# Performance work log

Hardware: AMD Instinct MI355X
Metric: run time of the kernel (lower is better)

The kernel has to match this reference:

```python
import jax, jax.numpy as jnp
import numpy as np

B, C, H, W = 8, 512, 64, 64
M = C // 8  # query/key channels (scale=8)
EPS = 1e-10
PARAM = 10.0


def elus_feature_map(t):
    # relu branch scaled by PARAM; exp(PARAM * negative part) - 1; +1
    pos = jax.nn.relu(t)
    neg = t - pos
    return PARAM * pos + (jnp.exp(PARAM * neg) - 1.0) + 1.0


def conv1x1(t_flat, Wc, bc):
    # t_flat: [B, Cin, N]; Wc: [Cout, Cin]; bc: [Cout]
    return jnp.einsum('oc,bcn->bon', Wc, t_flat) + bc[None, :, None]


def setup_inputs() -> dict:
    key = jax.random.key(0)
    ks = jax.random.split(key, 16)
    s_in = 1.0 / np.sqrt(C)
    d = dict(
        x=jax.random.normal(ks[0], (B, C, H, W), jnp.float32),
        y=jax.random.normal(ks[1], (B, C, H, W), jnp.float32),
        z=jax.random.normal(ks[2], (B, C, H, W), jnp.float32),
        Wq=jax.random.normal(ks[3], (M, C), jnp.float32) * s_in,
        bq=jnp.zeros((M,), jnp.float32),
        Wk1=jax.random.normal(ks[4], (M, C), jnp.float32) * s_in,
        bk1=jnp.zeros((M,), jnp.float32),
        Wk2=jax.random.normal(ks[5], (M, C), jnp.float32) * s_in,
        bk2=jnp.zeros((M,), jnp.float32),
        Wk3=jax.random.normal(ks[6], (M, C), jnp.float32) * s_in,
        bk3=jnp.zeros((M,), jnp.float32),
        Wv=jax.random.normal(ks[7], (C, C), jnp.float32) * s_in,
        bv=jnp.zeros((C,), jnp.float32),
        Wl=jax.random.normal(ks[8], (C, C), jnp.float32) * s_in,
        bl=jnp.zeros((C,), jnp.float32),
        gamma=jnp.zeros((1,), jnp.float32) + 0.5,  # nonzero so attention path is exercised
    )
    return d


def reference(x, y, z, Wq, bq, Wk1, bk1, Wk2, bk2, Wk3, bk3, Wv, bv, Wl, bl, gamma):
    N = H * W
    xf = x.reshape(B, C, N)
    yf = y.reshape(B, C, N)
    zf = z.reshape(B, C, N)

    Q = elus_feature_map(conv1x1(xf, Wq, bq))      # [B, M, N]
    K = elus_feature_map(conv1x1(xf, Wk1, bk1))    # [B, M, N]
    yK = elus_feature_map(conv1x1(yf, Wk2, bk2))   # [B, M, N]
    zK = elus_feature_map(conv1x1(zf, Wk3, bk3))   # [B, M, N]
    V = conv1x1(xf, Wv, bv)                        # [B, C, N]

    Qn = jnp.swapaxes(Q, 1, 2)                     # [B, N, M]

    def branch(Kb):
        KV = jnp.einsum('bmn,bcn->bmc', Kb, V)                      # [B, M, C]
        norm = 1.0 / jnp.einsum('bnm,bm->bn', Qn, Kb.sum(-1) + EPS)  # [B, N]
        return jnp.einsum('bnm,bmc,bn->bcn', Qn, KV, norm)          # [B, C, N]

    wv = branch(K) + branch(yK) + branch(zK)       # [B, C, N]
    attn = conv1x1(wv, Wl, bl).reshape(B, C, H, W)
    return x + gamma * attn
```

## Files before the change

### kernel.cpp

```cpp
#include <hip/hip_runtime.h>
#include <hip/hip_bf16.h>
#include <math.h>

constexpr int B_ = 8;
constexpr int C_ = 512;
constexpr int M_ = 64;
constexpr int N_ = 4096;
constexpr int NCHUNK_ = 4;
constexpr float EPS_ = 1e-10f;
constexpr float PARAM_ = 10.0f;

typedef __attribute__((ext_vector_type(4))) float f32x4;
typedef __attribute__((ext_vector_type(8))) short bf16x8;

__device__ __forceinline__ float elus(float t) {
    return (t > 0.f) ? fmaf(PARAM_, t, 1.f) : expf(PARAM_ * t);
}

__device__ __forceinline__ short f2bf(float f) {
    return __builtin_bit_cast(short, __float2bfloat16(f));
}
__device__ __forceinline__ float bf2f(short s) {
    unsigned u = ((unsigned)(unsigned short)s) << 16;
    return __builtin_bit_cast(float, u);
}

__global__ __launch_bounds__(256) void prep_w(const float* __restrict__ Wq,
                                              const float* __restrict__ Wk1,
                                              const float* __restrict__ Wk2,
                                              const float* __restrict__ Wk3,
                                              short* __restrict__ Wbf)
{
    int i = blockIdx.x * 256 + threadIdx.x;
    const int MC = M_ * C_;
    if (i < MC) {
        Wbf[i]          = f2bf(Wq[i]);
        Wbf[MC + i]     = f2bf(Wk1[i]);
        Wbf[2 * MC + i] = f2bf(Wk2[i]);
        Wbf[3 * MC + i] = f2bf(Wk3[i]);
    }
}

__global__ __launch_bounds__(256) void feat_mfma(
    const float* __restrict__ x, const float* __restrict__ y,
    const float* __restrict__ z, const short* __restrict__ Wbf,
    const float* __restrict__ bq, const float* __restrict__ bk1,
    const float* __restrict__ bk2, const float* __restrict__ bk3,
    short* __restrict__ QT, short* __restrict__ Kbuf3,
    float* __restrict__ Ksumpart)
{
    const int n0 = blockIdx.x * 64;
    const int which = blockIdx.y;
    const int b  = blockIdx.z;
    const int MC = M_ * C_;

    const float* in = (which == 0) ? x : (which == 1) ? y : z;
    const short* Ws0 = Wbf + (size_t)((which == 0) ? 0 : which + 1) * MC;
    const short* Ws1 = Wbf + (size_t)MC;

    __shared__ short Wlds[2][64][72];
    __shared__ short Xlds[64][72];

    const int tid  = threadIdx.x;
    const int lane = tid & 63;
    const int w    = tid >> 6;
    const int lrow = lane & 15;
    const int lkg  = lane >> 4;

    const float* inb = in + (size_t)b * C_ * N_;

    f32x4 accA[4] = {{0.f,0.f,0.f,0.f},{0.f,0.f,0.f,0.f},{0.f,0.f,0.f,0.f},{0.f,0.f,0.f,0.f}};
    f32x4 accB[4] = {{0.f,0.f,0.f,0.f},{0.f,0.f,0.f,0.f},{0.f,0.f,0.f,0.f},{0.f,0.f,0.f,0.f}};

    const int kq = tid >> 4;
    const int nq = tid & 15;

    for (int kc = 0; kc < C_ / 64; ++kc) {
        const int k0 = kc * 64;
        __syncthreads();
        #pragma unroll
        for (int i = 0; i < 2; ++i) {
            int f = tid + i * 256;
            int r = f >> 3, c8 = (f & 7) * 8;
            *reinterpret_cast<int4*>(&Wlds[0][r][c8]) =
                *reinterpret_cast<const int4*>(&Ws0[(size_t)r * C_ + k0 + c8]);
        }
        if (which == 0) {
            #pragma unroll
            for (int i = 0; i < 2; ++i) {
                int f = tid + i * 256;
                int r = f >> 3, c8 = (f & 7) * 8;
                *reinterpret_cast<int4*>(&Wlds[1][r][c8]) =
                    *reinterpret_cast<const int4*>(&Ws1[(size_t)r * C_ + k0 + c8]);
            }
        }
        f32x4 v0 = *reinterpret_cast<const f32x4*>(&inb[(size_t)(k0 + kq * 4 + 0) * N_ + n0 + nq * 4]);
        f32x4 v1 = *reinterpret_cast<const f32x4*>(&inb[(size_t)(k0 + kq * 4 + 1) * N_ + n0 + nq * 4]);
        f32x4 v2 = *reinterpret_cast<const f32x4*>(&inb[(size_t)(k0 + kq * 4 + 2) * N_ + n0 + nq * 4]);
        f32x4 v3 = *reinterpret_cast<const f32x4*>(&inb[(size_t)(k0 + kq * 4 + 3) * N_ + n0 + nq * 4]);
        #pragma unroll
        for (int c = 0; c < 4; ++c) {
            short4 s;
            s.x = f2bf(v0[c]); s.y = f2bf(v1[c]); s.z = f2bf(v2[c]); s.w = f2bf(v3[c]);
            *reinterpret_cast<short4*>(&Xlds[nq * 4 + c][kq * 4]) = s;
        }
        __syncthreads();
        #pragma unroll
        for (int ks = 0; ks < 2; ++ks) {
            bf16x8 a0 = *reinterpret_cast<const bf16x8*>(&Wlds[0][w * 16 + lrow][ks * 32 + lkg * 8]);
            bf16x8 a1;
            if (which == 0)
                a1 = *reinterpret_cast<const bf16x8*>(&Wlds[1][w * 16 + lrow][ks * 32 + lkg * 8]);
            #pragma unroll
            for (int ns = 0; ns < 4; ++ns) {
                bf16x8 bx = *reinterpret_cast<const bf16x8*>(&Xlds[ns * 16 + lrow][ks * 32 + lkg * 8]);
                accA[ns] = __builtin_amdgcn_mfma_f32_16x16x32_bf16(a0, bx, accA[ns], 0, 0, 0);
                if (which == 0)
                    accB[ns] = __builtin_amdgcn_mfma_f32_16x16x32_bf16(a1, bx, accB[ns], 0, 0, 0);
            }
        }
    }

    auto writeK = [&](const f32x4* acc, const float* bias, int br) {
        short* outb = Kbuf3 + ((size_t)br * B_ + b) * M_ * N_;
        float* ksp  = Ksumpart + ((size_t)br * B_ + b) * 64 * M_;
        #pragma unroll
        for (int r = 0; r < 4; ++r) {
            int m = w * 16 + lkg * 4 + r;
            float bi = bias[m];
            float sv = 0.f;
            #pragma unroll
            for (int ns = 0; ns < 4; ++ns) {
                int n = n0 + ns * 16 + lrow;
                float e = elus(acc[ns][r] + bi);
                outb[(size_t)m * N_ + n] = f2bf(e);
                sv += e;
            }
            sv += __shfl_xor(sv, 1);
            sv += __shfl_xor(sv, 2);
            sv += __shfl_xor(sv, 4);
            sv += __shfl_xor(sv, 8);
            if (lrow == 0)
                ksp[(size_t)blockIdx.x * M_ + m] = sv;
        }
    };

    if (which == 0) {
        short* outb = QT + (size_t)b * N_ * M_;
        int mbase = w * 16 + lkg * 4;
        float bi[4];
        #pragma unroll
        for (int r = 0; r < 4; ++r) bi[r] = bq[mbase + r];
        #pragma unroll
        for (int ns = 0; ns < 4; ++ns) {
            int n = n0 + ns * 16 + lrow;
            short4 s;
            s.x = f2bf(elus(accA[ns][0] + bi[0]));
            s.y = f2bf(elus(accA[ns][1] + bi[1]));
            s.z = f2bf(elus(accA[ns][2] + bi[2]));
            s.w = f2bf(elus(accA[ns][3] + bi[3]));
            *reinterpret_cast<short4*>(&outb[(size_t)n * M_ + mbase]) = s;
        }
        writeK(accB, bk1, 0);
    } else {
        writeK(accA, (which == 1) ? bk2 : bk3, which);
    }
}

__global__ __launch_bounds__(256) void ksum_finalize(const float* __restrict__ Ksumpart,
                                                     float* __restrict__ Ksum)
{
    int i = blockIdx.x * 256 + threadIdx.x;
    if (i >= 3 * B_ * M_) return;
    int br = i / (B_ * M_);
    int rem = i - br * (B_ * M_);
    int b = rem >> 6, m = rem & 63;
    const float* ksp = Ksumpart + ((size_t)br * B_ + b) * 64 * M_;
    float s = 0.f;
    #pragma unroll 8
    for (int nb = 0; nb < 64; ++nb) s += ksp[(size_t)nb * M_ + m];
    Ksum[((size_t)b * 3 + br) * M_ + m] = s;
}

__global__ __launch_bounds__(256) void kx3_mfma(const short* __restrict__ Kbuf3,
                                                const float* __restrict__ x,
                                                float* __restrict__ KXpart3)
{
    const int c0 = blockIdx.x * 32;
    const int nc = blockIdx.y;
    const int b  = blockIdx.z;
    const int nbeg = nc * (N_ / NCHUNK_);

    __shared__ short Klds[3][64][72];
    __shared__ short Xlds[32][72];

    const int tid  = threadIdx.x;
    const int lane = tid & 63;
    const int w    = tid >> 6;
    const int lrow = lane & 15;
    const int lkg  = lane >> 4;

    const float* xb = x + ((size_t)b * C_ + c0) * N_;

    f32x4 acc[3][2] = {};

    for (int it = 0; it < (N_ / NCHUNK_) / 64; ++it) {
        const int n0 = nbeg + it * 64;
        __syncthreads();
        #pragma unroll
        for (int br = 0; br < 3; ++br) {
            const short* kb = Kbuf3 + ((size_t)br * B_ + b) * M_ * N_;
            #pragma unroll
            for (int i = 0; i < 2; ++i) {
                int f = tid + i * 256;
                int r = f >> 3, c8 = (f & 7) * 8;
                *reinterpret_cast<int4*>(&Klds[br][r][c8]) =
                    *reinterpret_cast<const int4*>(&kb[(size_t)r * N_ + n0 + c8]);
            }
        }
        #pragma unroll
        for (int i = 0; i < 2; ++i) {
            int f = tid + i * 256;
            int r = f >> 4, c4 = (f & 15) * 4;
            float4 v = *reinterpret_cast<const float4*>(&xb[(size_t)r * N_ + n0 + c4]);
            short4 s;
            s.x = f2bf(v.x); s.y = f2bf(v.y); s.z = f2bf(v.z); s.w = f2bf(v.w);
            *reinterpret_cast<short4*>(&Xlds[r][c4]) = s;
        }
        __syncthreads();
        #pragma unroll
        for (int s = 0; s < 2; ++s) {
            bf16x8 b0 = *reinterpret_cast<const bf16x8*>(&Xlds[lrow][s * 32 + lkg * 8]);
            bf16x8 b1 = *reinterpret_cast<const bf16x8*>(&Xlds[16 + lrow][s * 32 + lkg * 8]);
            #pragma unroll
            for (int br = 0; br < 3; ++br) {
                bf16x8 a = *reinterpret_cast<const bf16x8*>(&Klds[br][w * 16 + lrow][s * 32 + lkg * 8]);
                acc[br][0] = __builtin_amdgcn_mfma_f32_16x16x32_bf16(a, b0, acc[br][0], 0, 0, 0);
                acc[br][1] = __builtin_amdgcn_mfma_f32_16x16x32_bf16(a, b1, acc[br][1], 0, 0, 0);
            }
        }
    }

    #pragma unroll
    for (int br = 0; br < 3; ++br) {
        float* outp = KXpart3 + (((size_t)br * NCHUNK_ + nc) * B_ + b) * M_ * C_;
        #pragma unroll
        for (int r = 0; r < 4; ++r) {
            int m = w * 16 + lkg * 4 + r;
            outp[(size_t)m * C_ + c0 + lrow]      = acc[br][0][r];
            outp[(size_t)m * C_ + c0 + 16 + lrow] = acc[br][1][r];
        }
    }
}

__global__ __launch_bounds__(256) void kx3_reduce(const float* __restrict__ KXpart3,
                                                  float* __restrict__ KX)
{
    const size_t BMC = (size_t)B_ * M_ * C_;
    size_t i = (size_t)blockIdx.x * 256 + threadIdx.x;
    if (i >= 3 * BMC) return;
    int br = (int)(i / BMC);
    size_t rem = i - (size_t)br * BMC;
    float s = 0.f;
    #pragma unroll
    for (int nc = 0; nc < NCHUNK_; ++nc)
        s += KXpart3[((size_t)br * NCHUNK_ + nc) * BMC + rem];
    size_t b = rem / ((size_t)M_ * C_);
    size_t mc = rem - b * (size_t)M_ * C_;
    KX[((size_t)b * 3 + br) * M_ * C_ + mc] = s;
}

__global__ __launch_bounds__(256) void wlwv_mfma(const float* __restrict__ Wl,
                                                 const float* __restrict__ Wv,
                                                 float* __restrict__ part)
{
    const int k0 = blockIdx.x * 64;
    const int c0 = blockIdx.y * 64;
    const int pc = blockIdx.z;

    __shared__ short Al[64][72];
    __shared__ short Bt[64][72];

    const int tid  = threadIdx.x;
    const int lane = tid & 63;
    const int w    = tid >> 6;
    const int lrow = lane & 15;
    const int lkg  = lane >> 4;
    const int pq = tid >> 4;
    const int nq = tid & 15;

    f32x4 acc[4] = {{0.f,0.f,0.f,0.f},{0.f,0.f,0.f,0.f},{0.f,0.f,0.f,0.f},{0.f,0.f,0.f,0.f}};

    for (int it = 0; it < 2; ++it) {
        const int p0 = pc * 128 + it * 64;
        __syncthreads();
        #pragma unroll
        for (int i = 0; i < 4; ++i) {
            int f = tid + i * 256;
            int r = f >> 4, c4 = (f & 15) * 4;
            f32x4 v = *reinterpret_cast<const f32x4*>(&Wl[(size_t)(c0 + r) * C_ + p0 + c4]);
            short4 s;
            s.x = f2bf(v[0]); s.y = f2bf(v[1]); s.z = f2bf(v[2]); s.w = f2bf(v[3]);
            *reinterpret_cast<short4*>(&Al[r][c4]) = s;
        }
        f32x4 v0 = *reinterpret_cast<const f32x4*>(&Wv[(size_t)(p0 + pq * 4 + 0) * C_ + k0 + nq * 4]);
        f32x4 v1 = *reinterpret_cast<const f32x4*>(&Wv[(size_t)(p0 + pq * 4 + 1) * C_ + k0 + nq * 4]);
        f32x4 v2 = *reinterpret_cast<const f32x4*>(&Wv[(size_t)(p0 + pq * 4 + 2) * C_ + k0 + nq * 4]);
        f32x4 v3 = *reinterpret_cast<const f32x4*>(&Wv[(size_t)(p0 + pq * 4 + 3) * C_ + k0 + nq * 4]);
        #pragma unroll
        for (int c = 0; c < 4; ++c) {
            short4 s;
            s.x = f2bf(v0[c]); s.y = f2bf(v1[c]); s.z = f2bf(v2[c]); s.w = f2bf(v3[c]);
            *reinterpret_cast<short4*>(&Bt[nq * 4 + c][pq * 4]) = s;
        }
        __syncthreads();
        #pragma unroll
        for (int ks = 0; ks < 2; ++ks) {
            bf16x8 a = *reinterpret_cast<const bf16x8*>(&Al[w * 16 + lrow][ks * 32 + lkg * 8]);
            #pragma unroll
            for (int ns = 0; ns < 4; ++ns) {
                bf16x8 bx = *reinterpret_cast<const bf16x8*>(&Bt[ns * 16 + lrow][ks * 32 + lkg * 8]);
                acc[ns] = __builtin_amdgcn_mfma_f32_16x16x32_bf16(a, bx, acc[ns], 0, 0, 0);
            }
        }
    }

    float* pp = part + (size_t)pc * C_ * C_;
    #pragma unroll
    for (int r = 0; r < 4; ++r) {
        int c = c0 + w * 16 + lkg * 4 + r;
        #pragma unroll
        for (int ns = 0; ns < 4; ++ns) {
            int k = k0 + ns * 16 + lrow;
            pp[(size_t)c * C_ + k] = acc[ns][r];
        }
    }
}

__global__ __launch_bounds__(256) void wlwv_reduce(const float* __restrict__ part,
                                                   float* __restrict__ WlWv)
{
    const size_t CC = (size_t)C_ * C_;
    size_t i = (size_t)blockIdx.x * 256 + threadIdx.x;
    if (i >= CC) return;
    float s = 0.f;
    #pragma unroll
    for (int pc = 0; pc < 4; ++pc) s += part[pc * CC + i];
    WlWv[i] = s;
}

__global__ __launch_bounds__(256) void wlbv_kernel(const float* __restrict__ Wl,
                                                   const float* __restrict__ bv,
                                                   float* __restrict__ Wlbv)
{
    int c = blockIdx.x * 256 + threadIdx.x;
    if (c < C_) {
        float s = 0.f;
        for (int p = 0; p < C_; ++p) s = fmaf(Wl[(size_t)c * C_ + p], bv[p], s);
        Wlbv[c] = s;
    }
}

__global__ __launch_bounds__(256) void wfused_mfma(const float* __restrict__ WlWv,
                                                   const float* __restrict__ KX,
                                                   const float* __restrict__ Ksum,
                                                   const float* __restrict__ Wlbv,
                                                   float* __restrict__ Wf)
{
    const int c0 = blockIdx.x * 64;
    const int br = blockIdx.y;
    const int b  = blockIdx.z;

    __shared__ short Al[64][72];
    __shared__ short Bl[64][72];

    const int tid  = threadIdx.x;
    const int lane = tid & 63;
    const int w    = tid >> 6;
    const int lrow = lane & 15;
    const int lkg  = lane >> 4;

    const float* kxb = KX + ((size_t)b * 3 + br) * M_ * C_;

    f32x4 acc[4] = {{0.f,0.f,0.f,0.f},{0.f,0.f,0.f,0.f},{0.f,0.f,0.f,0.f},{0.f,0.f,0.f,0.f}};

    for (int kc = 0; kc < C_ / 64; ++kc) {
        const int k0 = kc * 64;
        __syncthreads();
        #pragma unroll
        for (int i = 0; i < 4; ++i) {
            int f = tid + i * 256;
            int r = f >> 4, c4 = (f & 15) * 4;
            f32x4 v = *reinterpret_cast<const f32x4*>(&WlWv[(size_t)(c0 + r) * C_ + k0 + c4]);
            short4 s;
            s.x = f2bf(v[0]); s.y = f2bf(v[1]); s.z = f2bf(v[2]); s.w = f2bf(v[3]);
            *reinterpret_cast<short4*>(&Al[r][c4]) = s;
        }
        #pragma unroll
        for (int i = 0; i < 4; ++i) {
            int f = tid + i * 256;
            int r = f >> 4, c4 = (f & 15) * 4;
            f32x4 v = *reinterpret_cast<const f32x4*>(&kxb[(size_t)r * C_ + k0 + c4]);
            short4 s;
            s.x = f2bf(v[0]); s.y = f2bf(v[1]); s.z = f2bf(v[2]); s.w = f2bf(v[3]);
            *reinterpret_cast<short4*>(&Bl[r][c4]) = s;
        }
        __syncthreads();
        #pragma unroll
        for (int ks = 0; ks < 2; ++ks) {
            bf16x8 a = *reinterpret_cast<const bf16x8*>(&Al[w * 16 + lrow][ks * 32 + lkg * 8]);
            #pragma unroll
            for (int ns = 0; ns < 4; ++ns) {
                bf16x8 bx = *reinterpret_cast<const bf16x8*>(&Bl[ns * 16 + lrow][ks * 32 + lkg * 8]);
                acc[ns] = __builtin_amdgcn_mfma_f32_16x16x32_bf16(a, bx, acc[ns], 0, 0, 0);
            }
        }
    }

    const float* ks_ = Ksum + ((size_t)b * 3 + br) * M_;
    float* wfb = Wf + (((size_t)b * 3 + br) * C_) * M_;
    #pragma unroll
    for (int r = 0; r < 4; ++r) {
        int c = c0 + w * 16 + lkg * 4 + r;
        float wb = Wlbv[c];
        #pragma unroll
        for (int ns = 0; ns < 4; ++ns) {
            int m = ns * 16 + lrow;
            wfb[(size_t)c * M_ + m] = acc[ns][r] + ks_[m] * wb;
        }
    }
}

__global__ __launch_bounds__(256) void final_mfma_kernel(
    const short* __restrict__ QT, const float* __restrict__ Wf,
    const float* __restrict__ Ksum, const float* __restrict__ x,
    const float* __restrict__ bl, const float* __restrict__ gamma,
    float* __restrict__ out)
{
    const int n0 = blockIdx.x * 64;
    const int c0 = blockIdx.y * 64;
    const int b  = blockIdx.z;

    __shared__ short Qs[64][72];
    __shared__ short Wfs[3][64][72];
    __shared__ float norms[3][64];
    __shared__ float ksef[3][64];

    const int tid  = threadIdx.x;
    const int lane = tid & 63;
    const int w    = tid >> 6;
    const int lrow = lane & 15;
    const int lkg  = lane >> 4;

    const short* qtb = QT + (size_t)b * N_ * M_;
    #pragma unroll
    for (int i = 0; i < 2; ++i) {
        int f = tid + i * 256;
        int r = f >> 3, m8 = (f & 7) * 8;
        *reinterpret_cast<int4*>(&Qs[r][m8]) =
            *reinterpret_cast<const int4*>(&qtb[(size_t)(n0 + r) * M_ + m8]);
    }
    #pragma unroll
    for (int br = 0; br < 3; ++br) {
        const float* wfb = Wf + (((size_t)b * 3 + br) * C_ + c0) * M_;
        #pragma unroll
        for (int i = 0; i < 4; ++i) {
            int f = tid + i * 256;
            int r = f >> 4, m4 = (f & 15) * 4;
            float4 v = *reinterpret_cast<const float4*>(&wfb[(size_t)r * M_ + m4]);
            short4 s;
            s.x = f2bf(v.x); s.y = f2bf(v.y); s.z = f2bf(v.z); s.w = f2bf(v.w);
            *reinterpret_cast<short4*>(&Wfs[br][r][m4]) = s;
        }
    }
    if (tid < 192) {
        int br = tid >> 6, m = tid & 63;
        ksef[br][m] = Ksum[((size_t)b * 3 + br) * M_ + m] + EPS_;
    }
    __syncthreads();
    if (tid < 192) {
        int br = tid >> 6, n = tid & 63;
        float s = 0.f;
        #pragma unroll 16
        for (int m = 0; m < 64; ++m) s = fmaf(bf2f(Qs[n][m]), ksef[br][m], s);
        norms[br][n] = 1.0f / s;
    }
    __syncthreads();

    f32x4 tot[4] = {{0.f,0.f,0.f,0.f},{0.f,0.f,0.f,0.f},{0.f,0.f,0.f,0.f},{0.f,0.f,0.f,0.f}};
    for (int br = 0; br < 3; ++br) {
        f32x4 acc[4] = {{0.f,0.f,0.f,0.f},{0.f,0.f,0.f,0.f},{0.f,0.f,0.f,0.f},{0.f,0.f,0.f,0.f}};
        #pragma unroll
        for (int ks = 0; ks < 2; ++ks) {
            bf16x8 a = *reinterpret_cast<const bf16x8*>(&Wfs[br][w * 16 + lrow][ks * 32 + lkg * 8]);
            #pragma unroll
            for (int ns = 0; ns < 4; ++ns) {
                bf16x8 bq = *reinterpret_cast<const bf16x8*>(&Qs[ns * 16 + lrow][ks * 32 + lkg * 8]);
                acc[ns] = __builtin_amdgcn_mfma_f32_16x16x32_bf16(a, bq, acc[ns], 0, 0, 0);
            }
        }
        #pragma unroll
        for (int ns = 0; ns < 4; ++ns) {
            float nf = norms[br][ns * 16 + lrow];
            #pragma unroll
            for (int r = 0; r < 4; ++r) tot[ns][r] = fmaf(nf, acc[ns][r], tot[ns][r]);
        }
    }

    const float g = gamma[0];
    const float* xb = x + (size_t)b * C_ * N_;
    float* ob = out + (size_t)b * C_ * N_;
    #pragma unroll
    for (int r = 0; r < 4; ++r) {
        int c = c0 + w * 16 + lkg * 4 + r;
        float blc = bl[c];
        #pragma unroll
        for (int ns = 0; ns < 4; ++ns) {
            int n = n0 + ns * 16 + lrow;
            ob[(size_t)c * N_ + n] = fmaf(g, tot[ns][r] + blc, xb[(size_t)c * N_ + n]);
        }
    }
}

extern "C" void kernel_launch(void* const* d_in, const int* in_sizes, int n_in,
                              void* d_out, int out_size, void* d_ws, size_t ws_size,
                              hipStream_t stream)
{
    const float* x   = (const float*)d_in[0];
    const float* y   = (const float*)d_in[1];
    const float* z   = (const float*)d_in[2];
    const float* Wq  = (const float*)d_in[3];
    const float* bq  = (const float*)d_in[4];
    const float* Wk1 = (const float*)d_in[5];
    const float* bk1 = (const float*)d_in[6];
    const float* Wk2 = (const float*)d_in[7];
    const float* bk2 = (const float*)d_in[8];
    const float* Wk3 = (const float*)d_in[9];
    const float* bk3 = (const float*)d_in[10];
    const float* Wv  = (const float*)d_in[11];
    const float* bv  = (const float*)d_in[12];
    const float* Wl  = (const float*)d_in[13];
    const float* bl  = (const float*)d_in[14];
    const float* gamma = (const float*)d_in[15];
    float* out = (float*)d_out;

    float* ws = (float*)d_ws;
    const size_t QSZ  = (size_t)B_ * M_ * N_;
    const size_t BMC  = (size_t)B_ * M_ * C_;
    short* QTs   = (short*)ws;
    short* Kbuf3 = QTs + QSZ;
    float* fbase = ws + 2 * QSZ;
    float* KX    = fbase;
    float* Ksum  = KX + 3 * BMC;
    float* WlWv  = Ksum + (size_t)B_ * 3 * M_;
    float* Wlbv  = WlWv + (size_t)C_ * C_;
    float* Ksumpart = Wlbv + C_;
    float* KXpart3  = Ksumpart + (size_t)3 * B_ * 64 * M_;
    float* WlWvPart = KXpart3;
    float* Wf   = KXpart3;
    short* Wbf  = (short*)(KXpart3 + (size_t)3 * NCHUNK_ * BMC);

    dim3 blk(256);

    prep_w<<<dim3((M_ * C_ + 255) / 256), blk, 0, stream>>>(Wq, Wk1, Wk2, Wk3, Wbf);
    feat_mfma<<<dim3(N_ / 64, 3, B_), blk, 0, stream>>>(
        x, y, z, Wbf, bq, bk1, bk2, bk3, QTs, Kbuf3, Ksumpart);
    ksum_finalize<<<dim3((3 * B_ * M_ + 255) / 256), blk, 0, stream>>>(Ksumpart, Ksum);
    kx3_mfma<<<dim3(C_ / 32, NCHUNK_, B_), blk, 0, stream>>>(Kbuf3, x, KXpart3);
    kx3_reduce<<<dim3((int)((3 * BMC + 255) / 256)), blk, 0, stream>>>(KXpart3, KX);

    wlwv_mfma<<<dim3(C_ / 64, C_ / 64, 4), blk, 0, stream>>>(Wl, Wv, WlWvPart);
    wlwv_reduce<<<dim3(((int)((size_t)C_ * C_) + 255) / 256), blk, 0, stream>>>(WlWvPart, WlWv);
    wlbv_kernel<<<dim3((C_ + 255) / 256), blk, 0, stream>>>(Wl, bv, Wlbv);
    wfused_mfma<<<dim3(C_ / 64, 3, B_), blk, 0, stream>>>(WlWv, KX, Ksum, Wlbv, Wf);
    final_mfma_kernel<<<dim3(N_ / 64, C_ / 64, B_), blk, 0, stream>>>(
        QTs, Wf, Ksum, x, bl, gamma, out);
}
```

Baseline: 165.4 us.

## Prefetch next tile's global loads into registers during MFMA compute

```diff
diff --git a/kernel.cpp b/kernel.cpp
--- a/kernel.cpp
+++ b/kernel.cpp
@@ -74,37 +74,49 @@
 
     const int kq = tid >> 4;
     const int nq = tid & 15;
+    const int wr = tid >> 3, wc8 = (tid & 7) * 8;
+    const int wr2 = (tid + 256) >> 3, wc82 = ((tid + 256) & 7) * 8;
+
+    int4 wreg0a, wreg0b, wreg1a, wreg1b;
+    f32x4 xr0, xr1, xr2, xr3;
+
+    auto issueW = [&](int k0) {
+        wreg0a = *reinterpret_cast<const int4*>(&Ws0[(size_t)wr * C_ + k0 + wc8]);
+        wreg0b = *reinterpret_cast<const int4*>(&Ws0[(size_t)wr2 * C_ + k0 + wc82]);
+        if (which == 0) {
+            wreg1a = *reinterpret_cast<const int4*>(&Ws1[(size_t)wr * C_ + k0 + wc8]);
+            wreg1b = *reinterpret_cast<const int4*>(&Ws1[(size_t)wr2 * C_ + k0 + wc82]);
+        }
+    };
+    auto issueX = [&](int k0) {
+        xr0 = *reinterpret_cast<const f32x4*>(&inb[(size_t)(k0 + kq * 4 + 0) * N_ + n0 + nq * 4]);
+        xr1 = *reinterpret_cast<const f32x4*>(&inb[(size_t)(k0 + kq * 4 + 1) * N_ + n0 + nq * 4]);
+        xr2 = *reinterpret_cast<const f32x4*>(&inb[(size_t)(k0 + kq * 4 + 2) * N_ + n0 + nq * 4]);
+        xr3 = *reinterpret_cast<const f32x4*>(&inb[(size_t)(k0 + kq * 4 + 3) * N_ + n0 + nq * 4]);
+    };
+
+    issueW(0);
+    issueX(0);
 
     for (int kc = 0; kc < C_ / 64; ++kc) {
-        const int k0 = kc * 64;
-        __syncthreads();
-        #pragma unroll
-        for (int i = 0; i < 2; ++i) {
-            int f = tid + i * 256;
-            int r = f >> 3, c8 = (f & 7) * 8;
-            *reinterpret_cast<int4*>(&Wlds[0][r][c8]) =
-                *reinterpret_cast<const int4*>(&Ws0[(size_t)r * C_ + k0 + c8]);
-        }
+        __syncthreads();
+        *reinterpret_cast<int4*>(&Wlds[0][wr][wc8])   = wreg0a;
+        *reinterpret_cast<int4*>(&Wlds[0][wr2][wc82]) = wreg0b;
         if (which == 0) {
-            #pragma unroll
-            for (int i = 0; i < 2; ++i) {
-                int f = tid + i * 256;
-                int r = f >> 3, c8 = (f & 7) * 8;
-                *reinterpret_cast<int4*>(&Wlds[1][r][c8]) =
-                    *reinterpret_cast<const int4*>(&Ws1[(size_t)r * C_ + k0 + c8]);
-            }
-        }
-        f32x4 v0 = *reinterpret_cast<const f32x4*>(&inb[(size_t)(k0 + kq * 4 + 0) * N_ + n0 + nq * 4]);
-        f32x4 v1 = *reinterpret_cast<const f32x4*>(&inb[(size_t)(k0 + kq * 4 + 1) * N_ + n0 + nq * 4]);
-        f32x4 v2 = *reinterpret_cast<const f32x4*>(&inb[(size_t)(k0 + kq * 4 + 2) * N_ + n0 + nq * 4]);
-        f32x4 v3 = *reinterpret_cast<const f32x4*>(&inb[(size_t)(k0 + kq * 4 + 3) * N_ + n0 + nq * 4]);
+            *reinterpret_cast<int4*>(&Wlds[1][wr][wc8])   = wreg1a;
+            *reinterpret_cast<int4*>(&Wlds[1][wr2][wc82]) = wreg1b;
+        }
         #pragma unroll
         for (int c = 0; c < 4; ++c) {
             short4 s;
-            s.x = f2bf(v0[c]); s.y = f2bf(v1[c]); s.z = f2bf(v2[c]); s.w = f2bf(v3[c]);
+            s.x = f2bf(xr0[c]); s.y = f2bf(xr1[c]); s.z = f2bf(xr2[c]); s.w = f2bf(xr3[c]);
             *reinterpret_cast<short4*>(&Xlds[nq * 4 + c][kq * 4]) = s;
         }
         __syncthreads();
+        if (kc + 1 < C_ / 64) {
+            issueW((kc + 1) * 64);
+            issueX((kc + 1) * 64);
+        }
         #pragma unroll
         for (int ks = 0; ks < 2; ++ks) {
             bf16x8 a0 = *reinterpret_cast<const bf16x8*>(&Wlds[0][w * 16 + lrow][ks * 32 + lkg * 8]);
@@ -204,30 +216,50 @@
 
     f32x4 acc[3][2] = {};
 
+    const int kr1 = tid >> 3, kc81 = (tid & 7) * 8;
+    const int kr2 = (tid + 256) >> 3, kc82 = ((tid + 256) & 7) * 8;
+    const int xr1_ = tid >> 4, xc41 = (tid & 15) * 4;
+    const int xr2_ = (tid + 256) >> 4, xc42 = ((tid + 256) & 15) * 4;
+
+    int4 kreg[3][2];
+    float4 xrg0, xrg1;
+
+    auto issueK = [&](int n0) {
+        #pragma unroll
+        for (int br = 0; br < 3; ++br) {
+            const short* kb = Kbuf3 + ((size_t)br * B_ + b) * M_ * N_;
+            kreg[br][0] = *reinterpret_cast<const int4*>(&kb[(size_t)kr1 * N_ + n0 + kc81]);
+            kreg[br][1] = *reinterpret_cast<const int4*>(&kb[(size_t)kr2 * N_ + n0 + kc82]);
+        }
+    };
+    auto issueX = [&](int n0) {
+        xrg0 = *reinterpret_cast<const float4*>(&xb[(size_t)xr1_ * N_ + n0 + xc41]);
+        xrg1 = *reinterpret_cast<const float4*>(&xb[(size_t)xr2_ * N_ + n0 + xc42]);
+    };
+
+    issueK(nbeg);
+    issueX(nbeg);
+
     for (int it = 0; it < (N_ / NCHUNK_) / 64; ++it) {
         const int n0 = nbeg + it * 64;
         __syncthreads();
         #pragma unroll
         for (int br = 0; br < 3; ++br) {
-            const short* kb = Kbuf3 + ((size_t)br * B_ + b) * M_ * N_;
-            #pragma unroll
-            for (int i = 0; i < 2; ++i) {
-                int f = tid + i * 256;
-                int r = f >> 3, c8 = (f & 7) * 8;
-                *reinterpret_cast<int4*>(&Klds[br][r][c8]) =
-                    *reinterpret_cast<const int4*>(&kb[(size_t)r * N_ + n0 + c8]);
-            }
-        }
-        #pragma unroll
-        for (int i = 0; i < 2; ++i) {
-            int f = tid + i * 256;
-            int r = f >> 4, c4 = (f & 15) * 4;
-            float4 v = *reinterpret_cast<const float4*>(&xb[(size_t)r * N_ + n0 + c4]);
-            short4 s;
-            s.x = f2bf(v.x); s.y = f2bf(v.y); s.z = f2bf(v.z); s.w = f2bf(v.w);
-            *reinterpret_cast<short4*>(&Xlds[r][c4]) = s;
-        }
-        __syncthreads();
+            *reinterpret_cast<int4*>(&Klds[br][kr1][kc81]) = kreg[br][0];
+            *reinterpret_cast<int4*>(&Klds[br][kr2][kc82]) = kreg[br][1];
+        }
+        {
+            short4 s0, s1;
+            s0.x = f2bf(xrg0.x); s0.y = f2bf(xrg0.y); s0.z = f2bf(xrg0.z); s0.w = f2bf(xrg0.w);
+            s1.x = f2bf(xrg1.x); s1.y = f2bf(xrg1.y); s1.z = f2bf(xrg1.z); s1.w = f2bf(xrg1.w);
+            *reinterpret_cast<short4*>(&Xlds[xr1_][xc41]) = s0;
+            *reinterpret_cast<short4*>(&Xlds[xr2_][xc42]) = s1;
+        }
+        __syncthreads();
+        if (it + 1 < (N_ / NCHUNK_) / 64) {
+            issueK(n0 + 64);
+            issueX(n0 + 64);
+        }
         #pragma unroll
         for (int s = 0; s < 2; ++s) {
             bf16x8 b0 = *reinterpret_cast<const bf16x8*>(&Xlds[lrow][s * 32 + lkg * 8]);
```

Measured after the change: 205.4 us. 24.2% more time.
